# Kernel optimization log

Hardware: AMD Instinct MI355X
Metric: run time of the kernel (lower is better)

The kernel has to match this reference:

```python
import jax, jax.numpy as jnp
import numpy as np

N_NODE = 50000
N_EDGE = 625000
FDIM = 128
HID = 128
EPS = 1e-5


def setup_inputs() -> dict:
    key = jax.random.key(0)
    ks = jax.random.split(key, 12)
    node_feature = jax.random.normal(ks[0], (N_NODE, FDIM), dtype=jnp.float32)
    edge_matrix = jax.random.randint(ks[1], (2, N_EDGE), 0, N_NODE, dtype=jnp.int32)
    edge_feature = jax.random.normal(ks[2], (N_EDGE, FDIM), dtype=jnp.float32)
    in_dim = FDIM + FDIM  # concat(node, aggregated edge)
    s1 = 1.0 / np.sqrt(in_dim)
    s2 = 1.0 / np.sqrt(HID)
    W1 = jax.random.uniform(ks[3], (in_dim, HID), jnp.float32, -s1, s1)
    b1 = jax.random.uniform(ks[4], (HID,), jnp.float32, -s1, s1)
    W2 = jax.random.uniform(ks[5], (HID, HID), jnp.float32, -s2, s2)
    b2 = jax.random.uniform(ks[6], (HID,), jnp.float32, -s2, s2)
    W3 = jax.random.uniform(ks[7], (HID, FDIM), jnp.float32, -s2, s2)
    b3 = jax.random.uniform(ks[8], (FDIM,), jnp.float32, -s2, s2)
    gamma = jnp.ones((FDIM,), jnp.float32)
    beta = jnp.zeros((FDIM,), jnp.float32)
    return {"node_feature": node_feature, "edge_matrix": edge_matrix,
            "edge_feature": edge_feature, "W1": W1, "b1": b1, "W2": W2,
            "b2": b2, "W3": W3, "b3": b3, "gamma": gamma, "beta": beta}


def reference(node_feature, edge_matrix, edge_feature, W1, b1, W2, b2, W3, b3, gamma, beta):
    # receiver_idx = edge_matrix.T[:, 1] with edge_matrix [2, N_edge] -> row 1
    receiver_idx = edge_matrix[1]
    # scatter_add over receiver: [N_node, fdim]
    agg = jax.ops.segment_sum(edge_feature, receiver_idx, num_segments=node_feature.shape[0])
    x = jnp.concatenate([node_feature, agg], axis=-1)  # [N_node, 2*fdim]
    h = jax.nn.relu(x @ W1 + b1)
    h = jax.nn.relu(h @ W2 + b2)
    h = h @ W3 + b3
    # LayerNorm over last dim (eps = 1e-5, torch default)
    mu = jnp.mean(h, axis=-1, keepdims=True)
    var = jnp.mean((h - mu) ** 2, axis=-1, keepdims=True)
    h = (h - mu) * jax.lax.rsqrt(var + EPS) * gamma + beta
    return h + node_feature
```

## Files before the change

### kernel.cpp

```cpp
#include <hip/hip_runtime.h>
#include <hip/hip_bf16.h>

#define N_NODE 50000
#define N_EDGE 625000
#define FDIM 128
#define CAP 64

typedef __bf16 bf16x8 __attribute__((ext_vector_type(8)));
typedef float floatx4 __attribute__((ext_vector_type(4)));

#define MT 64
#define XS_LD 264
#define H_LD 136

__device__ inline bf16x8 as_bf16x8(uint4 v) {
    union { uint4 u; bf16x8 b; } c; c.u = v; return c.b;
}

__global__ __launch_bounds__(256) void wrepack_kernel(
    const float* __restrict__ W1, const float* __restrict__ W2,
    const float* __restrict__ W3, uint4* __restrict__ wp,
    int* __restrict__ count)
{
    if (blockIdx.x >= 32) {
        int idx = (blockIdx.x - 32) * 256 + threadIdx.x;
        for (int i = idx; i < N_NODE; i += 32 * 256) count[i] = 0;
        return;
    }
    int g = blockIdx.x * 256 + threadIdx.x;
    int lane = g & 63;
    int nt = (g >> 6) & 7;
    int tile = g >> 9;
    const float* W; int k0;
    if (tile < 8)       { W = W1; k0 = tile * 32; }
    else if (tile < 12) { W = W2; k0 = (tile - 8) * 32; }
    else                { W = W3; k0 = (tile - 12) * 32; }
    int n = nt * 16 + (lane & 15);
    int kb = k0 + (lane >> 4) * 8;
    union { __bf16 b[8]; uint4 u; } p;
#pragma unroll
    for (int j = 0; j < 8; ++j) p.b[j] = (__bf16)W[(kb + j) * 128 + n];
    wp[g] = p.u;
}

__global__ __launch_bounds__(256) void scatter_kernel(
    const int* __restrict__ recv, int* __restrict__ count, int* __restrict__ eid)
{
    int e = blockIdx.x * 256 + threadIdx.x;
    if (e < N_EDGE) {
        int r = recv[e];
        int p = atomicAdd(&count[r], 1);
        if (p < CAP) eid[(r << 6) + p] = e;
    }
}

__global__ __launch_bounds__(256) void gather_kernel(
    const float4* __restrict__ ef4, const int* __restrict__ count,
    const int* __restrict__ eid, uint2* __restrict__ agg)
{
    int wave = threadIdx.x >> 6;
    int lane = threadIdx.x & 63;
    int node = blockIdx.x * 4 + wave;
    int half = lane >> 5;
    int c = lane & 31;
    float4 acc = {0.f, 0.f, 0.f, 0.f};
    int cnt = count[node]; if (cnt > CAP) cnt = CAP;
    int ids = (lane < cnt) ? eid[(node << 6) + lane] : 0;
    int j = 0;
    for (; j + 8 <= cnt; j += 8) {
        int ea = __shfl(ids, j + half);
        int eb = __shfl(ids, j + 2 + half);
        int ec = __shfl(ids, j + 4 + half);
        int ed = __shfl(ids, j + 6 + half);
        float4 va = ef4[(long)ea * 32 + c];
        float4 vb = ef4[(long)eb * 32 + c];
        float4 vc = ef4[(long)ec * 32 + c];
        float4 vd = ef4[(long)ed * 32 + c];
        acc.x += va.x + vb.x + vc.x + vd.x;
        acc.y += va.y + vb.y + vc.y + vd.y;
        acc.z += va.z + vb.z + vc.z + vd.z;
        acc.w += va.w + vb.w + vc.w + vd.w;
    }
    if (j + 4 <= cnt) {
        int ea = __shfl(ids, j + half);
        int eb = __shfl(ids, j + 2 + half);
        float4 va = ef4[(long)ea * 32 + c];
        float4 vb = ef4[(long)eb * 32 + c];
        acc.x += va.x + vb.x; acc.y += va.y + vb.y;
        acc.z += va.z + vb.z; acc.w += va.w + vb.w;
        j += 4;
    }
    if (j + 2 <= cnt) {
        int e = __shfl(ids, j + half);
        float4 v = ef4[(long)e * 32 + c];
        acc.x += v.x; acc.y += v.y; acc.z += v.z; acc.w += v.w;
        j += 2;
    }
    if (j + half < cnt) {
        int e = __shfl(ids, j + half);
        float4 v = ef4[(long)e * 32 + c];
        acc.x += v.x; acc.y += v.y; acc.z += v.z; acc.w += v.w;
    }
    acc.x += __shfl_xor(acc.x, 32);
    acc.y += __shfl_xor(acc.y, 32);
    acc.z += __shfl_xor(acc.z, 32);
    acc.w += __shfl_xor(acc.w, 32);
    if (half == 0) {
        union { __bf16 b[4]; uint2 u; } p;
        p.b[0] = (__bf16)acc.x; p.b[1] = (__bf16)acc.y;
        p.b[2] = (__bf16)acc.z; p.b[3] = (__bf16)acc.w;
        agg[(long)node * 32 + c] = p.u;
    }
}

__global__ __launch_bounds__(256, 4) void mlp_kernel(
    const float* __restrict__ nodef, const int* __restrict__ agg32,
    const uint4* __restrict__ wp,
    const float* __restrict__ b1, const float* __restrict__ b2,
    const float* __restrict__ b3,
    const float* __restrict__ gamma, const float* __restrict__ beta,
    float* __restrict__ out)
{
    __shared__ __bf16 smem[17472];
    __bf16* xs = smem;
    __bf16* h1 = smem;
    __bf16* h2 = smem + 8704;

    const int t = threadIdx.x;
    const int wave = t >> 6;
    const int lane = t & 63;
    const int quad = lane >> 4;
    const int l16 = lane & 15;
    const int w16 = wave << 4;
    const int q8 = quad << 3;
    const int node0 = blockIdx.x * MT;

    const float4* nf4 = (const float4*)nodef;
#pragma unroll
    for (int i = 0; i < 8; ++i) {
        int it = i * 256 + t;
        int row = it >> 5;
        int c4 = it & 31;
        int node = node0 + row;
        if (node >= N_NODE) node = N_NODE - 1;
        float4 v = nf4[(long)node * 32 + c4];
        union { __bf16 b[4]; short4 s; } u;
        u.b[0] = (__bf16)v.x; u.b[1] = (__bf16)v.y;
        u.b[2] = (__bf16)v.z; u.b[3] = (__bf16)v.w;
        *(short4*)&xs[row * XS_LD + c4 * 4] = u.s;
    }
    const int4* ag4 = (const int4*)agg32;
#pragma unroll
    for (int i = 0; i < 4; ++i) {
        int it = i * 256 + t;
        int row = it >> 4;
        int c8 = it & 15;
        int node = node0 + row;
        if (node >= N_NODE) node = N_NODE - 1;
        int4 v = ag4[(long)node * 16 + c8];
        *(int4*)&xs[row * XS_LD + 128 + c8 * 8] = v;
    }

    floatx4 acc[8];
    const floatx4 zero = {0.f, 0.f, 0.f, 0.f};

    auto run_gemm = [&](const __bf16* A, int ldA, const uint4* __restrict__ wpt, int nk) {
#pragma unroll
        for (int nt = 0; nt < 8; ++nt) acc[nt] = zero;
        const __bf16* arow = A + (w16 + l16) * ldA + q8;
        bf16x8 a = *(const bf16x8*)arow;
        bf16x8 bA[4], bB[4];
#pragma unroll
        for (int i = 0; i < 4; ++i) bA[i] = as_bf16x8(wpt[i * 64 + lane]);
        for (int kc = 0; kc < nk; ++kc) {
            const uint4* wk = wpt + kc * 512;
#pragma unroll
            for (int i = 0; i < 4; ++i) bB[i] = as_bf16x8(wk[(4 + i) * 64 + lane]);
            bf16x8 a2 = a;
            if (kc + 1 < nk) a2 = *(const bf16x8*)(arow + (kc + 1) * 32);
#pragma unroll
            for (int nt = 0; nt < 4; ++nt)
                acc[nt] = __builtin_amdgcn_mfma_f32_16x16x32_bf16(a, bA[nt], acc[nt], 0, 0, 0);
            if (kc + 1 < nk) {
#pragma unroll
                for (int i = 0; i < 4; ++i) bA[i] = as_bf16x8(wk[512 + i * 64 + lane]);
            }
#pragma unroll
            for (int nt = 0; nt < 4; ++nt)
                acc[4 + nt] = __builtin_amdgcn_mfma_f32_16x16x32_bf16(a, bB[nt], acc[4 + nt], 0, 0, 0);
            a = a2;
        }
    };

    auto epilogue_relu = [&](const float* __restrict__ bias, __bf16* H) {
#pragma unroll
        for (int nt = 0; nt < 8; ++nt) {
            int col = nt * 16 + l16;
            float bv = bias[col];
#pragma unroll
            for (int r = 0; r < 4; ++r) {
                float v = acc[nt][r] + bv;
                v = v > 0.f ? v : 0.f;
                H[(w16 + quad * 4 + r) * H_LD + col] = (__bf16)v;
            }
        }
    };

    __syncthreads();
    run_gemm(xs, XS_LD, wp, 8);
    __syncthreads();
    epilogue_relu(b1, h1);
    __syncthreads();
    run_gemm(h1, H_LD, wp + 4096, 4);
    epilogue_relu(b2, h2);
    __syncthreads();
    run_gemm(h2, H_LD, wp + 6144, 4);

    float vout[8][4];
    float sum[4] = {0.f, 0.f, 0.f, 0.f};
    float sq[4]  = {0.f, 0.f, 0.f, 0.f};
#pragma unroll
    for (int nt = 0; nt < 8; ++nt) {
        int col = nt * 16 + l16;
        float bv = b3[col];
#pragma unroll
        for (int r = 0; r < 4; ++r) {
            float v = acc[nt][r] + bv;
            vout[nt][r] = v;
            sum[r] += v;
            sq[r] += v * v;
        }
    }
#pragma unroll
    for (int r = 0; r < 4; ++r) {
#pragma unroll
        for (int offs = 1; offs < 16; offs <<= 1) {
            sum[r] += __shfl_xor(sum[r], offs);
            sq[r]  += __shfl_xor(sq[r], offs);
        }
    }
    float mu[4], rs[4];
#pragma unroll
    for (int r = 0; r < 4; ++r) {
        mu[r] = sum[r] * (1.f / 128.f);
        float var = sq[r] * (1.f / 128.f) - mu[r] * mu[r];
        rs[r] = rsqrtf(var + 1e-5f);
    }
#pragma unroll
    for (int nt = 0; nt < 8; ++nt) {
        int col = nt * 16 + l16;
        float g = gamma[col], be = beta[col];
#pragma unroll
        for (int r = 0; r < 4; ++r) {
            int row = w16 + quad * 4 + r;
            int node = node0 + row;
            if (node < N_NODE) {
                long o = (long)node * 128 + col;
                out[o] = (vout[nt][r] - mu[r]) * rs[r] * g + be + nodef[o];
            }
        }
    }
}

extern "C" void kernel_launch(void* const* d_in, const int* in_sizes, int n_in,
                              void* d_out, int out_size, void* d_ws, size_t ws_size,
                              hipStream_t stream)
{
    const float* nodef = (const float*)d_in[0];
    const int*   em    = (const int*)d_in[1];
    const float* ef    = (const float*)d_in[2];
    const float* W1    = (const float*)d_in[3];
    const float* b1    = (const float*)d_in[4];
    const float* W2    = (const float*)d_in[5];
    const float* b2    = (const float*)d_in[6];
    const float* W3    = (const float*)d_in[7];
    const float* b3    = (const float*)d_in[8];
    const float* gamma = (const float*)d_in[9];
    const float* beta  = (const float*)d_in[10];
    float* out = (float*)d_out;

    int* count = (int*)d_ws;
    int* agg32 = count + 50048;
    uint4* wp  = (uint4*)(agg32 + 3200000);

    int* eid = (int*)d_out;

    const int* recv = em + N_EDGE;

    wrepack_kernel<<<64, 256, 0, stream>>>(W1, W2, W3, wp, count);

    int eblocks = (N_EDGE + 255) / 256;
    scatter_kernel<<<eblocks, 256, 0, stream>>>(recv, count, eid);
    gather_kernel<<<N_NODE / 4, 256, 0, stream>>>((const float4*)ef, count, eid, (uint2*)agg32);

    int mblocks = (N_NODE + MT - 1) / MT;
    mlp_kernel<<<mblocks, 256, 0, stream>>>(nodef, agg32, wp, b1, b2, b3,
                                            gamma, beta, out);
}
```

Before: 535.8 us.

## Fuse edge gather-aggregation into MLP kernel and drop separate gather pass

Removes the standalone gather kernel and performs the per-node edge-feature summation inside the MLP kernel. Each wave aggregates 16 nodes sequentially, prefetching the next node's count and edge IDs, and writes bf16 sums straight into the shared-memory input tile. This avoids one launch and the round trip of the aggregated buffer through global memory. The cost is that gather parallelism is now bound to the MLP kernel's occupancy (one wave per 16 nodes), which may hide less memory latency. The eid list moves from the output buffer into workspace.

```diff
diff --git a/kernel.cpp b/kernel.cpp
--- a/kernel.cpp
+++ b/kernel.cpp
@@ -54,67 +54,9 @@
     }
 }
 
-__global__ __launch_bounds__(256) void gather_kernel(
-    const float4* __restrict__ ef4, const int* __restrict__ count,
-    const int* __restrict__ eid, uint2* __restrict__ agg)
-{
-    int wave = threadIdx.x >> 6;
-    int lane = threadIdx.x & 63;
-    int node = blockIdx.x * 4 + wave;
-    int half = lane >> 5;
-    int c = lane & 31;
-    float4 acc = {0.f, 0.f, 0.f, 0.f};
-    int cnt = count[node]; if (cnt > CAP) cnt = CAP;
-    int ids = (lane < cnt) ? eid[(node << 6) + lane] : 0;
-    int j = 0;
-    for (; j + 8 <= cnt; j += 8) {
-        int ea = __shfl(ids, j + half);
-        int eb = __shfl(ids, j + 2 + half);
-        int ec = __shfl(ids, j + 4 + half);
-        int ed = __shfl(ids, j + 6 + half);
-        float4 va = ef4[(long)ea * 32 + c];
-        float4 vb = ef4[(long)eb * 32 + c];
-        float4 vc = ef4[(long)ec * 32 + c];
-        float4 vd = ef4[(long)ed * 32 + c];
-        acc.x += va.x + vb.x + vc.x + vd.x;
-        acc.y += va.y + vb.y + vc.y + vd.y;
-        acc.z += va.z + vb.z + vc.z + vd.z;
-        acc.w += va.w + vb.w + vc.w + vd.w;
-    }
-    if (j + 4 <= cnt) {
-        int ea = __shfl(ids, j + half);
-        int eb = __shfl(ids, j + 2 + half);
-        float4 va = ef4[(long)ea * 32 + c];
-        float4 vb = ef4[(long)eb * 32 + c];
-        acc.x += va.x + vb.x; acc.y += va.y + vb.y;
-        acc.z += va.z + vb.z; acc.w += va.w + vb.w;
-        j += 4;
-    }
-    if (j + 2 <= cnt) {
-        int e = __shfl(ids, j + half);
-        float4 v = ef4[(long)e * 32 + c];
-        acc.x += v.x; acc.y += v.y; acc.z += v.z; acc.w += v.w;
-        j += 2;
-    }
-    if (j + half < cnt) {
-        int e = __shfl(ids, j + half);
-        float4 v = ef4[(long)e * 32 + c];
-        acc.x += v.x; acc.y += v.y; acc.z += v.z; acc.w += v.w;
-    }
-    acc.x += __shfl_xor(acc.x, 32);
-    acc.y += __shfl_xor(acc.y, 32);
-    acc.z += __shfl_xor(acc.z, 32);
-    acc.w += __shfl_xor(acc.w, 32);
-    if (half == 0) {
-        union { __bf16 b[4]; uint2 u; } p;
-        p.b[0] = (__bf16)acc.x; p.b[1] = (__bf16)acc.y;
-        p.b[2] = (__bf16)acc.z; p.b[3] = (__bf16)acc.w;
-        agg[(long)node * 32 + c] = p.u;
-    }
-}
-
 __global__ __launch_bounds__(256, 4) void mlp_kernel(
-    const float* __restrict__ nodef, const int* __restrict__ agg32,
+    const float* __restrict__ nodef, const float4* __restrict__ ef4,
+    const int* __restrict__ count, const int* __restrict__ eid,
     const uint4* __restrict__ wp,
     const float* __restrict__ b1, const float* __restrict__ b2,
     const float* __restrict__ b3,
@@ -149,16 +91,70 @@
         u.b[2] = (__bf16)v.z; u.b[3] = (__bf16)v.w;
         *(short4*)&xs[row * XS_LD + c4 * 4] = u.s;
     }
-    const int4* ag4 = (const int4*)agg32;
-#pragma unroll
-    for (int i = 0; i < 4; ++i) {
-        int it = i * 256 + t;
-        int row = it >> 4;
-        int c8 = it & 15;
-        int node = node0 + row;
-        if (node >= N_NODE) node = N_NODE - 1;
-        int4 v = ag4[(long)node * 16 + c8];
-        *(int4*)&xs[row * XS_LD + 128 + c8 * 8] = v;
+
+    {
+        const int half = lane >> 5;
+        const int c = lane & 31;
+        const int n0r = node0 + (wave << 4);
+        int ncl = n0r < N_NODE ? n0r : N_NODE - 1;
+        int cnt = count[ncl]; if (cnt > CAP) cnt = CAP;
+        int ids = eid[(ncl << 6) + lane];
+        for (int i = 0; i < 16; ++i) {
+            int cnt_n = 0, ids_n = 0;
+            if (i < 15) {
+                int n1 = n0r + i + 1;
+                int ncl1 = n1 < N_NODE ? n1 : N_NODE - 1;
+                cnt_n = count[ncl1]; if (cnt_n > CAP) cnt_n = CAP;
+                ids_n = eid[(ncl1 << 6) + lane];
+            }
+            float4 acc = {0.f, 0.f, 0.f, 0.f};
+            int j = 0;
+            for (; j + 8 <= cnt; j += 8) {
+                int ea = __shfl(ids, j + half);
+                int eb = __shfl(ids, j + 2 + half);
+                int ec = __shfl(ids, j + 4 + half);
+                int ed = __shfl(ids, j + 6 + half);
+                float4 va = ef4[(long)ea * 32 + c];
+                float4 vb = ef4[(long)eb * 32 + c];
+                float4 vc = ef4[(long)ec * 32 + c];
+                float4 vd = ef4[(long)ed * 32 + c];
+                acc.x += va.x + vb.x + vc.x + vd.x;
+                acc.y += va.y + vb.y + vc.y + vd.y;
+                acc.z += va.z + vb.z + vc.z + vd.z;
+                acc.w += va.w + vb.w + vc.w + vd.w;
+            }
+            if (j + 4 <= cnt) {
+                int ea = __shfl(ids, j + half);
+                int eb = __shfl(ids, j + 2 + half);
+                float4 va = ef4[(long)ea * 32 + c];
+                float4 vb = ef4[(long)eb * 32 + c];
+                acc.x += va.x + vb.x; acc.y += va.y + vb.y;
+                acc.z += va.z + vb.z; acc.w += va.w + vb.w;
+                j += 4;
+            }
+            if (j + 2 <= cnt) {
+                int e = __shfl(ids, j + half);
+                float4 v = ef4[(long)e * 32 + c];
+                acc.x += v.x; acc.y += v.y; acc.z += v.z; acc.w += v.w;
+                j += 2;
+            }
+            if (j + half < cnt) {
+                int e = __shfl(ids, j + half);
+                float4 v = ef4[(long)e * 32 + c];
+                acc.x += v.x; acc.y += v.y; acc.z += v.z; acc.w += v.w;
+            }
+            acc.x += __shfl_xor(acc.x, 32);
+            acc.y += __shfl_xor(acc.y, 32);
+            acc.z += __shfl_xor(acc.z, 32);
+            acc.w += __shfl_xor(acc.w, 32);
+            if (half == 0) {
+                union { __bf16 b[4]; short4 s; } p;
+                p.b[0] = (__bf16)acc.x; p.b[1] = (__bf16)acc.y;
+                p.b[2] = (__bf16)acc.z; p.b[3] = (__bf16)acc.w;
+                *(short4*)&xs[((wave << 4) + i) * XS_LD + 128 + c * 4] = p.s;
+            }
+            cnt = cnt_n; ids = ids_n;
+        }
     }
 
     floatx4 acc[8];
@@ -280,10 +276,8 @@
     float* out = (float*)d_out;
 
     int* count = (int*)d_ws;
-    int* agg32 = count + 50048;
-    uint4* wp  = (uint4*)(agg32 + 3200000);
-
-    int* eid = (int*)d_out;
+    int* eid   = count + 50048;
+    uint4* wp  = (uint4*)(eid + 3200000);
 
     const int* recv = em + N_EDGE;
 
@@ -291,9 +285,8 @@
 
     int eblocks = (N_EDGE + 255) / 256;
     scatter_kernel<<<eblocks, 256, 0, stream>>>(recv, count, eid);
-    gather_kernel<<<N_NODE / 4, 256, 0, stream>>>((const float4*)ef, count, eid, (uint2*)agg32);
 
     int mblocks = (N_NODE + MT - 1) / MT;
-    mlp_kernel<<<mblocks, 256, 0, stream>>>(nodef, agg32, wp, b1, b2, b3,
-                                            gamma, beta, out);
-}
+    mlp_kernel<<<mblocks, 256, 0, stream>>>(nodef, (const float4*)ef, count, eid,
+                                            wp, b1, b2, b3, gamma, beta, out);
+}
```

Result: no change. 544.0 us (+1.5%).
